# Kernel tuning notes

Hardware: AMD Instinct MI355X
Metric: run time of the kernel (lower is better)

## Reference

```python
import jax, jax.numpy as jnp
import numpy as np

N = 50000      # nodes
E = 800000     # edges (before self loops)
IN_DIM = 256
HID = 64       # per-head hidden dim
HEADS = 4
NEG_SLOPE = 0.2


def setup_inputs() -> dict:
    key = jax.random.key(0)
    k1, k2, k3, k4, k5, k6 = jax.random.split(key, 6)
    x = jax.random.normal(k1, (N, IN_DIM), dtype=jnp.float32)
    edge_index = jax.random.randint(k2, (2, E), 0, N, dtype=jnp.int64)
    # GATConv params (PyG layout): lin weight, att_src, att_dst, bias
    W = jax.random.normal(k3, (IN_DIM, HEADS * HID), dtype=jnp.float32) / np.sqrt(IN_DIM)
    att_src = jax.random.normal(k4, (HEADS, HID), dtype=jnp.float32) / np.sqrt(HID)
    att_dst = jax.random.normal(k5, (HEADS, HID), dtype=jnp.float32) / np.sqrt(HID)
    bias = jnp.zeros((HEADS * HID,), dtype=jnp.float32)
    return {"x": x, "edge_index": edge_index, "W": W,
            "att_src": att_src, "att_dst": att_dst, "bias": bias}


def _gat_forward(x, edge_index, W, att_src, att_dst, bias):
    n = x.shape[0]
    # linear projection per head: [N, H, F]
    h = (x @ W).reshape(n, HEADS, HID)
    # per-node attention logits (computed once on nodes, then gathered)
    a_src = jnp.einsum('nhf,hf->nh', h, att_src)  # [N, H]
    a_dst = jnp.einsum('nhf,hf->nh', h, att_dst)  # [N, H]
    # add self loops (PyG default add_self_loops=True)
    loop = jnp.arange(n, dtype=edge_index.dtype)
    src = jnp.concatenate([edge_index[0], loop])  # [E+N]
    dst = jnp.concatenate([edge_index[1], loop])  # [E+N]
    # edge attention logits with LeakyReLU
    e = jax.nn.leaky_relu(a_src[src] + a_dst[dst], NEG_SLOPE)  # [E+N, H]
    # segment softmax over incoming edges of each destination node
    m = jax.ops.segment_max(e, dst, num_segments=n)            # [N, H]
    num = jnp.exp(e - m[dst])                                  # [E+N, H]
    denom = jax.ops.segment_sum(num, dst, num_segments=n)      # [N, H]
    alpha = num / denom[dst]                                   # [E+N, H]
    # scatter-aggregate weighted source features
    msg = alpha[:, :, None] * h[src]                           # [E+N, H, F]
    out = jax.ops.segment_sum(msg, dst, num_segments=n)        # [N, H, F]
    out = out.reshape(n, HEADS * HID) + bias
    # GraphEncoder.forward: ReLU then Dropout (dropout=0 -> identity)
    return jax.nn.relu(out)


def reference(x, edge_index, W, att_src, att_dst, bias):
    return _gat_forward(x, edge_index, W, att_src, att_dst, bias)
```

## Files before the change

kernel.cpp:

```cpp
#include <hip/hip_runtime.h>
#include <hip/hip_bf16.h>

#define N_NODES 50000
#define N_EDGES 800000
#define TOT_EDGES (N_EDGES + N_NODES)
#define IN_DIM 256
#define OUT_DIM 256
#define HEADS 4
#define NEG_SLOPE 0.2f
#define CAP 96

#define FBLK 256
#define NT   1563
#define LDS_STRIDE 264

typedef __bf16 bf16x8 __attribute__((ext_vector_type(8)));
typedef __bf16 bf16x4 __attribute__((ext_vector_type(4)));
typedef float f32x4 __attribute__((ext_vector_type(4)));

__device__ __forceinline__ float b2f(unsigned short u) {
    union { float f; unsigned int i; } v; v.i = ((unsigned int)u) << 16; return v.f;
}

struct Args {
    const float* x; const int* ei; const float* W;
    const float* att_s; const float* att_d; const float* bias;
    float* out;
    __bf16* Wt; __bf16* h; float* a_src; float* a_dst;
    int* counts; int* ell;
};

__global__ __launch_bounds__(256) void k_wt(Args A) {
    __shared__ __bf16 ts[64][72];
    const int t = threadIdx.x;
    for (int i = blockIdx.x * 256 + t; i < N_NODES; i += 16 * 256)
        A.counts[i] = 0;
    const int k0 = (blockIdx.x >> 2) * 64;
    const int n0 = (blockIdx.x & 3) * 64;
    const float4* __restrict__ w4 = (const float4*)A.W;
#pragma unroll
    for (int i = 0; i < 4; ++i) {
        int idx = i * 256 + t;
        int kk = idx >> 4;
        int c4 = idx & 15;
        float4 v = w4[(size_t)(k0 + kk) * 64 + (n0 >> 2) + c4];
        ts[c4 * 4 + 0][kk] = (__bf16)v.x;
        ts[c4 * 4 + 1][kk] = (__bf16)v.y;
        ts[c4 * 4 + 2][kk] = (__bf16)v.z;
        ts[c4 * 4 + 3][kk] = (__bf16)v.w;
    }
    __syncthreads();
#pragma unroll
    for (int i = 0; i < 2; ++i) {
        int idx = i * 256 + t;
        int n = idx >> 3;
        int c8 = idx & 7;
        *(bf16x8*)(A.Wt + (size_t)(n0 + n) * IN_DIM + k0 + c8 * 8) =
            *(const bf16x8*)&ts[n][c8 * 8];
    }
}

__global__ __launch_bounds__(512, 2) void k_gemm_fill(Args A) {
    __shared__ __bf16 xs[32 * LDS_STRIDE];
    __shared__ float  lg[2][8][32];
    const int t = threadIdx.x;

    if (blockIdx.x >= FBLK) {
        const int tile = blockIdx.x - FBLK;
        const int wave = t >> 6;
        const int lane = t & 63;
        const int cc   = lane & 15;
        const int quad = lane >> 4;
        const int n0   = wave * 32;
        const __bf16* __restrict__ Wt = A.Wt;
        const float4* __restrict__ x4 = (const float4*)A.x;

        bf16x8 Bf[8][2];
#pragma unroll
        for (int kk = 0; kk < 8; ++kk)
#pragma unroll
            for (int f = 0; f < 2; ++f)
                Bf[kk][f] = *(const bf16x8*)(Wt
                    + (size_t)(n0 + f * 16 + cc) * IN_DIM + kk * 32 + quad * 8);
        float as0 = A.att_s[n0 + cc], as1 = A.att_s[n0 + 16 + cc];
        float ad0 = A.att_d[n0 + cc], ad1 = A.att_d[n0 + 16 + cc];

        float4 st[4];
#pragma unroll
        for (int i = 0; i < 4; ++i) {
            int f = i * 512 + t;
            int row = f >> 6, c4 = f & 63;
            int grow = tile * 32 + row; if (grow >= N_NODES) grow = N_NODES - 1;
            st[i] = x4[(size_t)grow * 64 + c4];
        }
#pragma unroll
        for (int i = 0; i < 4; ++i) {
            int f = i * 512 + t;
            int row = f >> 6, c4 = f & 63;
            bf16x4 o = { (__bf16)st[i].x, (__bf16)st[i].y, (__bf16)st[i].z, (__bf16)st[i].w };
            *(bf16x4*)&xs[row * LDS_STRIDE + c4 * 4] = o;
        }
        __syncthreads();

        f32x4 acc[2][2];
#pragma unroll
        for (int mt = 0; mt < 2; ++mt)
#pragma unroll
            for (int f = 0; f < 2; ++f) acc[mt][f] = (f32x4){0.f, 0.f, 0.f, 0.f};
#pragma unroll
        for (int kk = 0; kk < 8; ++kk) {
#pragma unroll
            for (int mt = 0; mt < 2; ++mt) {
                bf16x8 a = *(const bf16x8*)&xs[(mt * 16 + cc) * LDS_STRIDE + kk * 32 + quad * 8];
                acc[mt][0] = __builtin_amdgcn_mfma_f32_16x16x32_bf16(a, Bf[kk][0], acc[mt][0], 0, 0, 0);
                acc[mt][1] = __builtin_amdgcn_mfma_f32_16x16x32_bf16(a, Bf[kk][1], acc[mt][1], 0, 0, 0);
            }
        }

#pragma unroll
        for (int mt = 0; mt < 2; ++mt) {
#pragma unroll
            for (int r = 0; r < 4; ++r) {
                float pS = acc[mt][0][r] * as0 + acc[mt][1][r] * as1;
                float pD = acc[mt][0][r] * ad0 + acc[mt][1][r] * ad1;
#pragma unroll
                for (int o = 8; o >= 1; o >>= 1) {
                    pS += __shfl_xor(pS, o, 64);
                    pD += __shfl_xor(pD, o, 64);
                }
                if (cc == 0) {
                    lg[0][wave][mt * 16 + quad * 4 + r] = pS;
                    lg[1][wave][mt * 16 + quad * 4 + r] = pD;
                }
            }
        }
        __syncthreads();

#pragma unroll
        for (int mt = 0; mt < 2; ++mt)
#pragma unroll
            for (int f = 0; f < 2; ++f)
#pragma unroll
                for (int r = 0; r < 4; ++r)
                    xs[(mt * 16 + quad * 4 + r) * LDS_STRIDE + n0 + f * 16 + cc] =
                        (__bf16)acc[mt][f][r];
        if (t < 256) {
            int td = t & 127;
            int row = td >> 2, head = td & 3;
            int grow = tile * 32 + row;
            if (grow < N_NODES) {
                int sd = t >> 7;
                float v = lg[sd][2 * head][row] + lg[sd][2 * head + 1][row];
                float* dst = sd == 0 ? A.a_src : A.a_dst;
                dst[grow * 4 + head] = v;
            }
        }
        __syncthreads();

#pragma unroll
        for (int i = 0; i < 2; ++i) {
            int idx = i * 512 + t;
            int row = idx >> 5, c8 = idx & 31;
            int grow = tile * 32 + row;
            if (grow < N_NODES)
                *(bf16x8*)(A.h + (size_t)grow * OUT_DIM + c8 * 8) =
                    *(const bf16x8*)&xs[row * LDS_STRIDE + c8 * 8];
        }
    } else {
        int nz = 0;
        for (int i = t; i < 1024; i += 512)
            if (A.ei[2 * i + 1] != 0) nz++;
        bool is64 = (__syncthreads_count(nz) == 0);
        const long long* ei64 = (const long long*)A.ei;
        for (int i = blockIdx.x * 512 + t; i < TOT_EDGES; i += FBLK * 512) {
            int s, d;
            if (i < N_EDGES) {
                if (is64) { s = (int)ei64[i]; d = (int)ei64[N_EDGES + i]; }
                else      { s = A.ei[i];      d = A.ei[N_EDGES + i]; }
            } else {
                s = d = i - N_EDGES;
            }
            int pos = atomicAdd(&A.counts[d], 1);
            if (pos < CAP) A.ell[(size_t)d * CAP + pos] = s;
        }
    }
}

__global__ __launch_bounds__(256) void k_agg(Args A) {
    __shared__ float lds_all[4][CAP][4];
    int wave = threadIdx.x >> 6, lane = threadIdx.x & 63;
    int node = blockIdx.x * 4 + wave;
    if (node >= N_NODES) return;
    float (*lds)[4] = lds_all[wave];

    int base = node * CAP;
    int deg  = A.counts[node];
    if (deg > CAP) deg = CAP;
    const float4* as4 = (const float4*)A.a_src;
    float4 ad = ((const float4*)A.a_dst)[node];

    float4 smv = {0.f, 0.f, 0.f, 0.f};
    for (int e = lane; e < deg; e += 64) {
        int s = A.ell[base + e];
        float4 av = as4[s];
        float4 l;
        l.x = av.x + ad.x; l.x = l.x > 0.f ? l.x : NEG_SLOPE * l.x;
        l.y = av.y + ad.y; l.y = l.y > 0.f ? l.y : NEG_SLOPE * l.y;
        l.z = av.z + ad.z; l.z = l.z > 0.f ? l.z : NEG_SLOPE * l.z;
        l.w = av.w + ad.w; l.w = l.w > 0.f ? l.w : NEG_SLOPE * l.w;
        float4 e4;
        e4.x = __expf(l.x); e4.y = __expf(l.y);
        e4.z = __expf(l.z); e4.w = __expf(l.w);
        smv.x += e4.x; smv.y += e4.y; smv.z += e4.z; smv.w += e4.w;
        lds[e][0] = e4.x; lds[e][1] = e4.y; lds[e][2] = e4.z; lds[e][3] = e4.w;
    }
    int padEnd = (deg + 7) & ~7;
    for (int e = deg + lane; e < padEnd; e += 64) {
        lds[e][0] = 0.f; lds[e][1] = 0.f; lds[e][2] = 0.f; lds[e][3] = 0.f;
    }
#pragma unroll
    for (int o = 32; o >= 1; o >>= 1) {
        smv.x += __shfl_xor(smv.x, o, 64);
        smv.y += __shfl_xor(smv.y, o, 64);
        smv.z += __shfl_xor(smv.z, o, 64);
        smv.w += __shfl_xor(smv.w, o, 64);
    }

    int head = lane >> 4;
    float smh = head == 0 ? smv.x : head == 1 ? smv.y : head == 2 ? smv.z : smv.w;
    float inv_d = 1.f / smh;

    float acc0 = 0.f, acc1 = 0.f, acc2 = 0.f, acc3 = 0.f;
    const unsigned short* hs = reinterpret_cast<const unsigned short*>(A.h);
    for (int e = 0; e < padEnd; e += 8) {
        int si[8];
        float al[8];
        ushort4 hv[8];
#pragma unroll
        for (int j = 0; j < 8; ++j) {
            si[j] = A.ell[base + ((e + j < deg) ? e + j : 0)];
            al[j] = lds[e + j][head];
        }
#pragma unroll
        for (int j = 0; j < 8; ++j)
            hv[j] = *(const ushort4*)(hs + (size_t)si[j] * OUT_DIM + lane * 4);
#pragma unroll
        for (int j = 0; j < 8; ++j) {
            acc0 += al[j] * b2f(hv[j].x);
            acc1 += al[j] * b2f(hv[j].y);
            acc2 += al[j] * b2f(hv[j].z);
            acc3 += al[j] * b2f(hv[j].w);
        }
    }

    float4 bv = ((const float4*)A.bias)[lane];
    f32x4 o4;
    float v0 = acc0 * inv_d + bv.x;
    float v1 = acc1 * inv_d + bv.y;
    float v2 = acc2 * inv_d + bv.z;
    float v3 = acc3 * inv_d + bv.w;
    o4[0] = v0 > 0.f ? v0 : 0.f;
    o4[1] = v1 > 0.f ? v1 : 0.f;
    o4[2] = v2 > 0.f ? v2 : 0.f;
    o4[3] = v3 > 0.f ? v3 : 0.f;
    __builtin_nontemporal_store(o4, (f32x4*)A.out + (size_t)node * 64 + lane);
}

extern "C" void kernel_launch(void* const* d_in, const int* in_sizes, int n_in,
                              void* d_out, int out_size, void* d_ws, size_t ws_size,
                              hipStream_t stream) {
    (void)out_size; (void)ws_size;
    const void* p_x = nullptr; const void* p_ei = nullptr; const void* p_W = nullptr;
    const void* p_small[3] = {nullptr, nullptr, nullptr}; int nsmall = 0;
    for (int i = 0; i < n_in; ++i) {
        switch (in_sizes[i]) {
            case N_NODES * IN_DIM:      p_x = d_in[i]; break;
            case 2 * N_EDGES:           p_ei = d_in[i]; break;
            case IN_DIM * OUT_DIM:      p_W = d_in[i]; break;
            case OUT_DIM:               if (nsmall < 3) p_small[nsmall++] = d_in[i]; break;
            default: break;
        }
    }
    if (!p_x)  p_x  = d_in[0];
    if (!p_ei) p_ei = d_in[1];
    if (!p_W)  p_W  = d_in[2];
    if (nsmall < 3) { p_small[0] = d_in[3]; p_small[1] = d_in[4]; p_small[2] = d_in[5]; }

    char* ws = (char*)d_ws;
    size_t off = 0;
    auto alloc = [&](size_t bytes) -> void* {
        void* p = ws + off;
        off = (off + bytes + 255) & ~(size_t)255;
        return p;
    };
    Args A;
    A.Wt      = (__bf16*)alloc((size_t)IN_DIM * OUT_DIM * 2);
    A.h       = (__bf16*)alloc((size_t)N_NODES * OUT_DIM * 2);
    A.a_src   = (float*)alloc((size_t)N_NODES * HEADS * 4);
    A.a_dst   = (float*)alloc((size_t)N_NODES * HEADS * 4);
    A.counts  = (int*)alloc((size_t)N_NODES * 4);
    A.ell     = (int*)alloc((size_t)N_NODES * CAP * 4);

    A.x     = (const float*)p_x;
    A.ei    = (const int*)p_ei;
    A.W     = (const float*)p_W;
    A.att_s = (const float*)p_small[0];
    A.att_d = (const float*)p_small[1];
    A.bias  = (const float*)p_small[2];
    A.out   = (float*)d_out;

    k_wt<<<dim3(16), dim3(256), 0, stream>>>(A);
    k_gemm_fill<<<dim3(FBLK + NT), dim3(512), 0, stream>>>(A);
    k_agg<<<dim3((N_NODES + 3) / 4), dim3(256), 0, stream>>>(A);
}
```

Baseline: 238.5 us.

## Move edge fill into W-transpose kernel and split GEMM into own launch

Edge bucketing now runs in the same launch as the weight transpose, with one edge per thread across 1661 blocks instead of a grid-stride loop over 256 blocks. The GEMM becomes a standalone kernel, and the counts zeroing moves to a hipMemsetAsync. The aim is to spread the atomic-heavy fill across many more blocks and to stop it sharing blocks with the GEMM. In exchange it adds a memset and one more serialized kernel boundary, and the GEMM no longer overlaps the fill.

```diff
diff --git a/kernel.cpp b/kernel.cpp
--- a/kernel.cpp
+++ b/kernel.cpp
@@ -10,7 +10,8 @@
 #define NEG_SLOPE 0.2f
 #define CAP 96
 
-#define FBLK 256
+#define WTB  16
+#define FB2  1661
 #define NT   1563
 #define LDS_STRIDE 264
 
@@ -30,159 +31,156 @@
     int* counts; int* ell;
 };
 
-__global__ __launch_bounds__(256) void k_wt(Args A) {
+__global__ __launch_bounds__(512) void k_wt_fill(Args A) {
     __shared__ __bf16 ts[64][72];
     const int t = threadIdx.x;
-    for (int i = blockIdx.x * 256 + t; i < N_NODES; i += 16 * 256)
-        A.counts[i] = 0;
-    const int k0 = (blockIdx.x >> 2) * 64;
-    const int n0 = (blockIdx.x & 3) * 64;
-    const float4* __restrict__ w4 = (const float4*)A.W;
-#pragma unroll
-    for (int i = 0; i < 4; ++i) {
-        int idx = i * 256 + t;
-        int kk = idx >> 4;
-        int c4 = idx & 15;
-        float4 v = w4[(size_t)(k0 + kk) * 64 + (n0 >> 2) + c4];
-        ts[c4 * 4 + 0][kk] = (__bf16)v.x;
-        ts[c4 * 4 + 1][kk] = (__bf16)v.y;
-        ts[c4 * 4 + 2][kk] = (__bf16)v.z;
-        ts[c4 * 4 + 3][kk] = (__bf16)v.w;
-    }
-    __syncthreads();
-#pragma unroll
-    for (int i = 0; i < 2; ++i) {
-        int idx = i * 256 + t;
-        int n = idx >> 3;
-        int c8 = idx & 7;
-        *(bf16x8*)(A.Wt + (size_t)(n0 + n) * IN_DIM + k0 + c8 * 8) =
-            *(const bf16x8*)&ts[n][c8 * 8];
-    }
-}
-
-__global__ __launch_bounds__(512, 2) void k_gemm_fill(Args A) {
+
+    if (blockIdx.x < WTB) {
+        const int k0 = (blockIdx.x >> 2) * 64;
+        const int n0 = (blockIdx.x & 3) * 64;
+        const float4* __restrict__ w4 = (const float4*)A.W;
+#pragma unroll
+        for (int i = 0; i < 2; ++i) {
+            int idx = i * 512 + t;
+            int kk = idx >> 4;
+            int c4 = idx & 15;
+            float4 v = w4[(size_t)(k0 + kk) * 64 + (n0 >> 2) + c4];
+            ts[c4 * 4 + 0][kk] = (__bf16)v.x;
+            ts[c4 * 4 + 1][kk] = (__bf16)v.y;
+            ts[c4 * 4 + 2][kk] = (__bf16)v.z;
+            ts[c4 * 4 + 3][kk] = (__bf16)v.w;
+        }
+        __syncthreads();
+        {
+            int n = t >> 3;
+            int c8 = t & 7;
+            *(bf16x8*)(A.Wt + (size_t)(n0 + n) * IN_DIM + k0 + c8 * 8) =
+                *(const bf16x8*)&ts[n][c8 * 8];
+        }
+    } else {
+        int nz = 0;
+        for (int j = t; j < 1024; j += 512)
+            if (A.ei[2 * j + 1] != 0) nz++;
+        bool is64 = (__syncthreads_count(nz) == 0);
+        const long long* ei64 = (const long long*)A.ei;
+        int i = (blockIdx.x - WTB) * 512 + t;
+        if (i < N_EDGES) {
+            int s, d;
+            if (is64) { s = (int)ei64[i]; d = (int)ei64[N_EDGES + i]; }
+            else      { s = A.ei[i];      d = A.ei[N_EDGES + i]; }
+            int pos = atomicAdd(&A.counts[d], 1);
+            if (pos < CAP) A.ell[(size_t)d * CAP + pos] = s;
+        } else if (i < TOT_EDGES) {
+            int n = i - N_EDGES;
+            int pos = atomicAdd(&A.counts[n], 1);
+            if (pos < CAP) A.ell[(size_t)n * CAP + pos] = n;
+        }
+    }
+}
+
+__global__ __launch_bounds__(512, 2) void k_gemm(Args A) {
     __shared__ __bf16 xs[32 * LDS_STRIDE];
     __shared__ float  lg[2][8][32];
     const int t = threadIdx.x;
-
-    if (blockIdx.x >= FBLK) {
-        const int tile = blockIdx.x - FBLK;
-        const int wave = t >> 6;
-        const int lane = t & 63;
-        const int cc   = lane & 15;
-        const int quad = lane >> 4;
-        const int n0   = wave * 32;
-        const __bf16* __restrict__ Wt = A.Wt;
-        const float4* __restrict__ x4 = (const float4*)A.x;
-
-        bf16x8 Bf[8][2];
-#pragma unroll
-        for (int kk = 0; kk < 8; ++kk)
-#pragma unroll
-            for (int f = 0; f < 2; ++f)
-                Bf[kk][f] = *(const bf16x8*)(Wt
-                    + (size_t)(n0 + f * 16 + cc) * IN_DIM + kk * 32 + quad * 8);
-        float as0 = A.att_s[n0 + cc], as1 = A.att_s[n0 + 16 + cc];
-        float ad0 = A.att_d[n0 + cc], ad1 = A.att_d[n0 + 16 + cc];
-
-        float4 st[4];
-#pragma unroll
-        for (int i = 0; i < 4; ++i) {
-            int f = i * 512 + t;
-            int row = f >> 6, c4 = f & 63;
-            int grow = tile * 32 + row; if (grow >= N_NODES) grow = N_NODES - 1;
-            st[i] = x4[(size_t)grow * 64 + c4];
-        }
-#pragma unroll
-        for (int i = 0; i < 4; ++i) {
-            int f = i * 512 + t;
-            int row = f >> 6, c4 = f & 63;
-            bf16x4 o = { (__bf16)st[i].x, (__bf16)st[i].y, (__bf16)st[i].z, (__bf16)st[i].w };
-            *(bf16x4*)&xs[row * LDS_STRIDE + c4 * 4] = o;
-        }
-        __syncthreads();
-
-        f32x4 acc[2][2];
-#pragma unroll
-        for (int mt = 0; mt < 2; ++mt)
-#pragma unroll
-            for (int f = 0; f < 2; ++f) acc[mt][f] = (f32x4){0.f, 0.f, 0.f, 0.f};
-#pragma unroll
-        for (int kk = 0; kk < 8; ++kk) {
-#pragma unroll
-            for (int mt = 0; mt < 2; ++mt) {
-                bf16x8 a = *(const bf16x8*)&xs[(mt * 16 + cc) * LDS_STRIDE + kk * 32 + quad * 8];
-                acc[mt][0] = __builtin_amdgcn_mfma_f32_16x16x32_bf16(a, Bf[kk][0], acc[mt][0], 0, 0, 0);
-                acc[mt][1] = __builtin_amdgcn_mfma_f32_16x16x32_bf16(a, Bf[kk][1], acc[mt][1], 0, 0, 0);
+    const int tile = blockIdx.x;
+    const int wave = t >> 6;
+    const int lane = t & 63;
+    const int cc   = lane & 15;
+    const int quad = lane >> 4;
+    const int n0   = wave * 32;
+    const __bf16* __restrict__ Wt = A.Wt;
+    const float4* __restrict__ x4 = (const float4*)A.x;
+
+    bf16x8 Bf[8][2];
+#pragma unroll
+    for (int kk = 0; kk < 8; ++kk)
+#pragma unroll
+        for (int f = 0; f < 2; ++f)
+            Bf[kk][f] = *(const bf16x8*)(Wt
+                + (size_t)(n0 + f * 16 + cc) * IN_DIM + kk * 32 + quad * 8);
+    float as0 = A.att_s[n0 + cc], as1 = A.att_s[n0 + 16 + cc];
+    float ad0 = A.att_d[n0 + cc], ad1 = A.att_d[n0 + 16 + cc];
+
+    float4 st[4];
+#pragma unroll
+    for (int i = 0; i < 4; ++i) {
+        int f = i * 512 + t;
+        int row = f >> 6, c4 = f & 63;
+        int grow = tile * 32 + row; if (grow >= N_NODES) grow = N_NODES - 1;
+        st[i] = x4[(size_t)grow * 64 + c4];
+    }
+#pragma unroll
+    for (int i = 0; i < 4; ++i) {
+        int f = i * 512 + t;
+        int row = f >> 6, c4 = f & 63;
+        bf16x4 o = { (__bf16)st[i].x, (__bf16)st[i].y, (__bf16)st[i].z, (__bf16)st[i].w };
+        *(bf16x4*)&xs[row * LDS_STRIDE + c4 * 4] = o;
+    }
+    __syncthreads();
+
+    f32x4 acc[2][2];
+#pragma unroll
+    for (int mt = 0; mt < 2; ++mt)
+#pragma unroll
+        for (int f = 0; f < 2; ++f) acc[mt][f] = (f32x4){0.f, 0.f, 0.f, 0.f};
+#pragma unroll
+    for (int kk = 0; kk < 8; ++kk) {
+#pragma unroll
+        for (int mt = 0; mt < 2; ++mt) {
+            bf16x8 a = *(const bf16x8*)&xs[(mt * 16 + cc) * LDS_STRIDE + kk * 32 + quad * 8];
+            acc[mt][0] = __builtin_amdgcn_mfma_f32_16x16x32_bf16(a, Bf[kk][0], acc[mt][0], 0, 0, 0);
+            acc[mt][1] = __builtin_amdgcn_mfma_f32_16x16x32_bf16(a, Bf[kk][1], acc[mt][1], 0, 0, 0);
+        }
+    }
+
+#pragma unroll
+    for (int mt = 0; mt < 2; ++mt) {
+#pragma unroll
+        for (int r = 0; r < 4; ++r) {
+            float pS = acc[mt][0][r] * as0 + acc[mt][1][r] * as1;
+            float pD = acc[mt][0][r] * ad0 + acc[mt][1][r] * ad1;
+#pragma unroll
+            for (int o = 8; o >= 1; o >>= 1) {
+                pS += __shfl_xor(pS, o, 64);
+                pD += __shfl_xor(pD, o, 64);
             }
-        }
-
-#pragma unroll
-        for (int mt = 0; mt < 2; ++mt) {
-#pragma unroll
-            for (int r = 0; r < 4; ++r) {
-                float pS = acc[mt][0][r] * as0 + acc[mt][1][r] * as1;
-                float pD = acc[mt][0][r] * ad0 + acc[mt][1][r] * ad1;
-#pragma unroll
-                for (int o = 8; o >= 1; o >>= 1) {
-                    pS += __shfl_xor(pS, o, 64);
-                    pD += __shfl_xor(pD, o, 64);
-                }
-                if (cc == 0) {
-                    lg[0][wave][mt * 16 + quad * 4 + r] = pS;
-                    lg[1][wave][mt * 16 + quad * 4 + r] = pD;
-                }
+            if (cc == 0) {
+                lg[0][wave][mt * 16 + quad * 4 + r] = pS;
+                lg[1][wave][mt * 16 + quad * 4 + r] = pD;
             }
         }
-        __syncthreads();
-
-#pragma unroll
-        for (int mt = 0; mt < 2; ++mt)
-#pragma unroll
-            for (int f = 0; f < 2; ++f)
-#pragma unroll
-                for (int r = 0; r < 4; ++r)
-                    xs[(mt * 16 + quad * 4 + r) * LDS_STRIDE + n0 + f * 16 + cc] =
-                        (__bf16)acc[mt][f][r];
-        if (t < 256) {
-            int td = t & 127;
-            int row = td >> 2, head = td & 3;
-            int grow = tile * 32 + row;
-            if (grow < N_NODES) {
-                int sd = t >> 7;
-                float v = lg[sd][2 * head][row] + lg[sd][2 * head + 1][row];
-                float* dst = sd == 0 ? A.a_src : A.a_dst;
-                dst[grow * 4 + head] = v;
-            }
-        }
-        __syncthreads();
-
-#pragma unroll
-        for (int i = 0; i < 2; ++i) {
-            int idx = i * 512 + t;
-            int row = idx >> 5, c8 = idx & 31;
-            int grow = tile * 32 + row;
-            if (grow < N_NODES)
-                *(bf16x8*)(A.h + (size_t)grow * OUT_DIM + c8 * 8) =
-                    *(const bf16x8*)&xs[row * LDS_STRIDE + c8 * 8];
-        }
-    } else {
-        int nz = 0;
-        for (int i = t; i < 1024; i += 512)
-            if (A.ei[2 * i + 1] != 0) nz++;
-        bool is64 = (__syncthreads_count(nz) == 0);
-        const long long* ei64 = (const long long*)A.ei;
-        for (int i = blockIdx.x * 512 + t; i < TOT_EDGES; i += FBLK * 512) {
-            int s, d;
-            if (i < N_EDGES) {
-                if (is64) { s = (int)ei64[i]; d = (int)ei64[N_EDGES + i]; }
-                else      { s = A.ei[i];      d = A.ei[N_EDGES + i]; }
-            } else {
-                s = d = i - N_EDGES;
-            }
-            int pos = atomicAdd(&A.counts[d], 1);
-            if (pos < CAP) A.ell[(size_t)d * CAP + pos] = s;
-        }
+    }
+    __syncthreads();
+
+#pragma unroll
+    for (int mt = 0; mt < 2; ++mt)
+#pragma unroll
+        for (int f = 0; f < 2; ++f)
+#pragma unroll
+            for (int r = 0; r < 4; ++r)
+                xs[(mt * 16 + quad * 4 + r) * LDS_STRIDE + n0 + f * 16 + cc] =
+                    (__bf16)acc[mt][f][r];
+    if (t < 256) {
+        int td = t & 127;
+        int row = td >> 2, head = td & 3;
+        int grow = tile * 32 + row;
+        if (grow < N_NODES) {
+            int sd = t >> 7;
+            float v = lg[sd][2 * head][row] + lg[sd][2 * head + 1][row];
+            float* dst = sd == 0 ? A.a_src : A.a_dst;
+            dst[grow * 4 + head] = v;
+        }
+    }
+    __syncthreads();
+
+#pragma unroll
+    for (int i = 0; i < 2; ++i) {
+        int idx = i * 512 + t;
+        int row = idx >> 5, c8 = idx & 31;
+        int grow = tile * 32 + row;
+        if (grow < N_NODES)
+            *(bf16x8*)(A.h + (size_t)grow * OUT_DIM + c8 * 8) =
+                *(const bf16x8*)&xs[row * LDS_STRIDE + c8 * 8];
     }
 }
 
@@ -309,7 +307,8 @@
     A.bias  = (const float*)p_small[2];
     A.out   = (float*)d_out;
 
-    k_wt<<<dim3(16), dim3(256), 0, stream>>>(A);
-    k_gemm_fill<<<dim3(FBLK + NT), dim3(512), 0, stream>>>(A);
+    hipMemsetAsync(A.counts, 0, (size_t)N_NODES * 4, stream);
+    k_wt_fill<<<dim3(WTB + FB2), dim3(512), 0, stream>>>(A);
+    k_gemm<<<dim3(NT), dim3(512), 0, stream>>>(A);
     k_agg<<<dim3((N_NODES + 3) / 4), dim3(256), 0, stream>>>(A);
 }
```

After: 249.9 us. 4.8% more time.
